# Kernel optimization log

Measured on AMD Instinct MI355X. Metric: run time of the kernel, lower is better.

Reference implementation:

```python
import jax, jax.numpy as jnp
import numpy as np

N_HEAD = 16
MA_K = 0.02          # sigmoid temperature in ma_k_activation
LEAKY_SLOPE = 0.02   # negative_slope in ma_q_activation
NEG_INF = -1e9


def setup_inputs() -> dict:
    key = jax.random.key(0)
    k1, k2, k3, k4 = jax.random.split(key, 4)
    B, T, C = 2, 2048, 1024
    x = jax.random.normal(k1, (B, T, C), dtype=jnp.float32)
    s = 1.0 / np.sqrt(C)
    W_attn = jax.random.normal(k2, (C, 2 * C), dtype=jnp.float32) * s
    W_k2 = jax.random.normal(k3, (C, C), dtype=jnp.float32) * s
    W_proj = jax.random.normal(k4, (C, C), dtype=jnp.float32) * s
    return {"x": x, "W_attn": W_attn, "W_k2": W_k2, "W_proj": W_proj}


def _heads(t, H):
    # [B,T,C] -> [B,H,T,d]
    B, T, C = t.shape
    return t.reshape(B, T, H, C // H).transpose(0, 2, 1, 3)


def reference(x, W_attn, W_k2, W_proj):
    B, T, C = x.shape
    H = N_HEAD
    d = C // H
    scale = 1.0 / jnp.sqrt(jnp.asarray(d, x.dtype))

    qk = x @ W_attn                      # [B,T,2C]
    q, k = jnp.split(qk, 2, axis=-1)
    q = _heads(q, H)                     # [B,H,T,d]
    k = _heads(k, H)
    v = _heads(x, H)                     # v = x

    # --- AR branch: causal softmax attention ---
    scores = jnp.einsum('bhtd,bhsd->bhts', q, k) * scale
    causal = jnp.tril(jnp.ones((T, T), dtype=bool))
    scores = jnp.where(causal, scores, NEG_INF)
    attn = jax.nn.softmax(scores, axis=-1)
    y = jnp.einsum('bhts,bhsd->bhtd', attn, v)   # [B,H,T,d]

    # --- MA branch: causal, softmax-free linear attention on residual ---
    e = v[:, :, 1:, :] - y[:, :, :-1, :]          # [B,H,T-1,d]
    k2 = _heads(x[:, :-1, :] @ W_k2, H)           # [B,H,T-1,d]
    q2 = q[:, :, 1:, :]                           # [B,H,T-1,d]

    qa = -jax.nn.leaky_relu(-q2 * scale, negative_slope=LEAKY_SLOPE)
    ka = jax.nn.sigmoid(MA_K * (k2 * scale))

    w = jnp.einsum('bhtd,bhsd->bhts', qa, ka)     # [B,H,T-1,T-1]
    w = jnp.tril(w)
    y2 = jnp.einsum('bhts,bhsd->bhtd', w, e)      # [B,H,T-1,d]
    y2 = jnp.concatenate([jnp.zeros_like(y2[:, :, :1, :]), y2], axis=2)  # pad front

    def merge(t):  # [B,H,T,d] -> [B,T,C]
        return t.transpose(0, 2, 1, 3).reshape(B, T, C)

    return merge(y) @ W_proj + merge(y2) @ W_proj
```

## Files before the change

### kernel.cpp

```cpp
#include <hip/hip_runtime.h>

typedef unsigned short u16;
typedef u16   u16x4  __attribute__((ext_vector_type(4)));
typedef u16   u16x8  __attribute__((ext_vector_type(8)));
typedef __bf16 bf16x8 __attribute__((ext_vector_type(8)));
typedef float  f32x4  __attribute__((ext_vector_type(4)));

__device__ __forceinline__ float bf2f(u16 v) {
    unsigned u = ((unsigned)v) << 16;
    return __builtin_bit_cast(float, u);
}
__device__ __forceinline__ u16 f2bf(float f) {
    unsigned u = __builtin_bit_cast(unsigned, f);
    u += 0x7fffu + ((u >> 16) & 1u);
    return (u16)(u >> 16);
}

__device__ __forceinline__ void async16(const u16* g, u16* l) {
    __builtin_amdgcn_global_load_lds(
        (const __attribute__((address_space(1))) unsigned int*)g,
        (__attribute__((address_space(3))) unsigned int*)l,
        16, 0, 0);
}

__device__ __forceinline__ size_t kimg_idx(int bh, int s, int d) {
    return ((size_t)(bh * 32 + (s >> 6)) * 4096) + (size_t)(((d >> 3) * 64 + (s & 63)) * 8) + (d & 7);
}
__device__ __forceinline__ size_t vimg_idx(int bh, int s, int d) {
    return ((size_t)(bh * 32 + (s >> 6)) * 4096) + (size_t)((((s & 63) >> 3) * 64 + d) * 8) + (s & 7);
}

__global__ __launch_bounds__(256)
void convert_pack(const float* __restrict__ in, u16* __restrict__ xb,
                  u16* __restrict__ xpack) {
    int i = blockIdx.x * 256 + threadIdx.x;
    int c4 = i & 255, row = i >> 8;
    int s = row & 2047, b = row >> 11;
    float4 v = ((const float4*)in)[i];
    u16x4 o;
    o.x = f2bf(v.x); o.y = f2bf(v.y); o.z = f2bf(v.z); o.w = f2bf(v.w);
    ((u16x4*)xb)[i] = o;
    int h = c4 >> 4, d0 = (c4 & 15) * 4;
    size_t base = vimg_idx(b * 16 + h, s, d0);
    xpack[base]      = o.x;
    xpack[base + 8]  = o.y;
    xpack[base + 16] = o.z;
    xpack[base + 24] = o.w;
}

__global__ __launch_bounds__(256)
void prep_weights(const float* __restrict__ Wa, const float* __restrict__ Wk,
                  const float* __restrict__ Wp, u16* __restrict__ Wta,
                  u16* __restrict__ Wtk, u16* __restrict__ Wtp) {
    __shared__ u16 tile[64][65];
    const int bx = blockIdx.x;
    const float* in; u16* out; int Cd, cx;
    if (bx < 32)      { in = Wa; out = Wta; Cd = 2048; cx = bx; }
    else if (bx < 48) { in = Wk; out = Wtk; Cd = 1024; cx = bx - 32; }
    else              { in = Wp; out = Wtp; Cd = 1024; cx = bx - 48; }
    const int c0 = cx * 64, r0 = blockIdx.y * 64;
    const int tid = threadIdx.x;
#pragma unroll
    for (int i = 0; i < 16; ++i) {
        int idx = tid + i * 256;
        int r = idx >> 6, c = idx & 63;
        tile[r][c] = f2bf(in[(size_t)(r0 + r) * Cd + c0 + c]);
    }
    __syncthreads();
#pragma unroll
    for (int i = 0; i < 16; ++i) {
        int idx = tid + i * 256;
        int r = idx >> 6, c = idx & 63;
        out[(size_t)(c0 + r) * 1024 + r0 + c] = tile[c][r];
    }
}

__global__ __launch_bounds__(256, 3)
void gemm_fused(const u16* __restrict__ A, const u16* __restrict__ Bt,
                u16* __restrict__ qs, u16* __restrict__ kpack,
                u16* __restrict__ kapack) {
    const int K = 1024;
    __shared__ __align__(16) u16 As[4][128][8];
    __shared__ __align__(16) u16 Bs[4][128][8];
    const int tid = threadIdx.x;
    const int wave = tid >> 6, lane = tid & 63;
    const int m0 = blockIdx.y * 128, n0 = blockIdx.x * 128;
    const int wm = (wave >> 1) * 64, wn = (wave & 1) * 64;
    const int q = lane >> 4, mr = lane & 15;

    const int s0 = tid, s1 = 256 + tid;
    const u16* gA0 = A  + (size_t)(m0 + (s0 & 127)) * K + (s0 >> 7) * 8;
    const u16* gA1 = A  + (size_t)(m0 + (s1 & 127)) * K + (s1 >> 7) * 8;
    const u16* gB0 = Bt + (size_t)(n0 + (s0 & 127)) * K + (s0 >> 7) * 8;
    const u16* gB1 = Bt + (size_t)(n0 + (s1 & 127)) * K + (s1 >> 7) * 8;
    u16* lA0 = &As[0][0][0] + (size_t)s0 * 8;
    u16* lA1 = &As[0][0][0] + (size_t)s1 * 8;
    u16* lB0 = &Bs[0][0][0] + (size_t)s0 * 8;
    u16* lB1 = &Bs[0][0][0] + (size_t)s1 * 8;

    f32x4 acc[4][4];
#pragma unroll
    for (int i = 0; i < 4; ++i)
#pragma unroll
        for (int j = 0; j < 4; ++j) acc[i][j] = f32x4{0.f, 0.f, 0.f, 0.f};

    for (int k0 = 0; k0 < K; k0 += 32) {
        __syncthreads();
        async16(gA0 + k0, lA0);
        async16(gA1 + k0, lA1);
        async16(gB0 + k0, lB0);
        async16(gB1 + k0, lB1);
        asm volatile("s_waitcnt vmcnt(0)" ::: "memory");
        __syncthreads();
        bf16x8 af[4], bfr[4];
#pragma unroll
        for (int i = 0; i < 4; ++i) af[i]  = *(const bf16x8*)&As[q][wm + i * 16 + mr][0];
#pragma unroll
        for (int j = 0; j < 4; ++j) bfr[j] = *(const bf16x8*)&Bs[q][wn + j * 16 + mr][0];
#pragma unroll
        for (int i = 0; i < 4; ++i)
#pragma unroll
            for (int j = 0; j < 4; ++j)
                acc[i][j] = __builtin_amdgcn_mfma_f32_16x16x32_bf16(af[i], bfr[j], acc[i][j], 0, 0, 0);
    }
#pragma unroll
    for (int i = 0; i < 4; ++i)
#pragma unroll
        for (int j = 0; j < 4; ++j)
#pragma unroll
            for (int r = 0; r < 4; ++r) {
                int m = m0 + wm + i * 16 + q * 4 + r;
                int n = n0 + wn + j * 16 + mr;
                float v = acc[i][j][r];
                int b = m >> 11, s = m & 2047;
                if (n < 1024) {
                    qs[(size_t)m * 1024 + n] = f2bf(v * 0.125f);
                } else if (n < 2048) {
                    int nn = n - 1024;
                    kpack[kimg_idx(b * 16 + (nn >> 6), s, nn & 63)] = f2bf(v);
                } else {
                    int nn = n - 2048;
                    kapack[kimg_idx(b * 16 + (nn >> 6), s, nn & 63)] =
                        f2bf(1.f / (1.f + __expf(-0.0025f * v)));
                }
            }
}

__global__ __launch_bounds__(256, 2)
void gemm64(const u16* __restrict__ A, const u16* __restrict__ Bt,
            float* __restrict__ Cv, int N, int K) {
    __shared__ __align__(16) u16 As[4][64][8];
    __shared__ __align__(16) u16 Bs[4][128][8];
    const int tid = threadIdx.x;
    const int wave = tid >> 6, lane = tid & 63;
    const int m0 = blockIdx.y * 64, n0 = blockIdx.x * 128;
    const int wn0 = wave * 32;
    const int q = lane >> 4, mr = lane & 15;

    const u16* gA = A + (size_t)(m0 + (tid & 63)) * K + (tid >> 6) * 8;
    u16* lA = &As[0][0][0] + (size_t)tid * 8;
    const int s1 = 256 + tid;
    const u16* gB0 = Bt + (size_t)(n0 + (tid & 127)) * K + (tid >> 7) * 8;
    const u16* gB1 = Bt + (size_t)(n0 + (s1 & 127)) * K + (s1 >> 7) * 8;
    u16* lB0 = &Bs[0][0][0] + (size_t)tid * 8;
    u16* lB1 = &Bs[0][0][0] + (size_t)s1 * 8;

    f32x4 acc[4][2];
#pragma unroll
    for (int i = 0; i < 4; ++i)
#pragma unroll
        for (int j = 0; j < 2; ++j) acc[i][j] = f32x4{0.f, 0.f, 0.f, 0.f};

    for (int k0 = 0; k0 < K; k0 += 32) {
        __syncthreads();
        async16(gA + k0, lA);
        async16(gB0 + k0, lB0);
        async16(gB1 + k0, lB1);
        asm volatile("s_waitcnt vmcnt(0)" ::: "memory");
        __syncthreads();
        bf16x8 af[4], bfr[2];
#pragma unroll
        for (int i = 0; i < 4; ++i) af[i]  = *(const bf16x8*)&As[q][i * 16 + mr][0];
#pragma unroll
        for (int j = 0; j < 2; ++j) bfr[j] = *(const bf16x8*)&Bs[q][wn0 + j * 16 + mr][0];
#pragma unroll
        for (int i = 0; i < 4; ++i)
#pragma unroll
            for (int j = 0; j < 2; ++j)
                acc[i][j] = __builtin_amdgcn_mfma_f32_16x16x32_bf16(af[i], bfr[j], acc[i][j], 0, 0, 0);
    }
#pragma unroll
    for (int i = 0; i < 4; ++i)
#pragma unroll
        for (int j = 0; j < 2; ++j)
#pragma unroll
            for (int r = 0; r < 4; ++r) {
                int m = m0 + i * 16 + q * 4 + r;
                int n = n0 + wn0 + j * 16 + mr;
                Cv[(size_t)m * N + n] = acc[i][j][r];
            }
}

__global__ __launch_bounds__(256, 2)
void flash_mfma(const u16* __restrict__ qs, const u16* __restrict__ kpack,
                const u16* __restrict__ xpack, u16* __restrict__ Opart,
                float* __restrict__ lpart) {
    __shared__ __align__(16) u16 Ks[8][64][8];
    __shared__ __align__(16) u16 Vs[8][64][8];
    __shared__ __align__(16) u16 Ps[4][16][72];
    const int bh = blockIdx.y, b = bh >> 4, hc = (bh & 15) * 64;
    const int z = blockIdx.z;
    const int tid = threadIdx.x, w = tid >> 6, lane = tid & 63;
    const int n16 = lane & 15, quad = lane >> 4;
    const u16* kbase = kpack + (size_t)bh * 32 * 4096;
    const u16* vbase = xpack + (size_t)bh * 32 * 4096;
    u16* Ob = Opart + (size_t)z * 4096 * 1024;
    float* lb = lpart + z * 65536;

    for (int rep = 0; rep < 2; ++rep) {
        const int T = rep ? 15 - (int)blockIdx.x : (int)blockIdx.x;
        const int t0 = T * 128;
        const int nchunk = 2 * T + 2;

        bf16x8 qf[2][2];
#pragma unroll
        for (int mt = 0; mt < 2; ++mt) {
            const int trow = t0 + (w + mt * 4) * 16 + n16;
            const u16* qp = &qs[(size_t)(b * 2048 + trow) * 1024 + hc + quad * 8];
            qf[mt][0] = *(const bf16x8*)qp;
            qf[mt][1] = *(const bf16x8*)(qp + 32);
        }

        f32x4 O[2][4];
        float lsum[2][4];
#pragma unroll
        for (int mt = 0; mt < 2; ++mt)
#pragma unroll
            for (int jt = 0; jt < 4; ++jt) { O[mt][jt] = f32x4{0.f, 0.f, 0.f, 0.f}; }
#pragma unroll
        for (int mt = 0; mt < 2; ++mt)
#pragma unroll
            for (int r = 0; r < 4; ++r) lsum[mt][r] = 0.f;

        u16x8 kr0, kr1, vr0, vr1;
        auto pref = [&](int c) {
            const u16* kc = kbase + (size_t)c * 4096;
            const u16* vc = vbase + (size_t)c * 4096;
            kr0 = *(const u16x8*)(kc + tid * 8);
            kr1 = *(const u16x8*)(kc + (256 + tid) * 8);
            vr0 = *(const u16x8*)(vc + tid * 8);
            vr1 = *(const u16x8*)(vc + (256 + tid) * 8);
        };
        if (z < nchunk) pref(z);

        for (int c = z; c < nchunk; c += 2) {
            __syncthreads();
            *(u16x8*)((u16*)Ks + tid * 8)         = kr0;
            *(u16x8*)((u16*)Ks + (256 + tid) * 8) = kr1;
            *(u16x8*)((u16*)Vs + tid * 8)         = vr0;
            *(u16x8*)((u16*)Vs + (256 + tid) * 8) = vr1;
            __syncthreads();
            if (c + 2 < nchunk) pref(c + 2);

            f32x4 S[2][4];
#pragma unroll
            for (int mt = 0; mt < 2; ++mt)
#pragma unroll
                for (int jt = 0; jt < 4; ++jt) S[mt][jt] = f32x4{0.f, 0.f, 0.f, 0.f};
#pragma unroll
            for (int ks = 0; ks < 2; ++ks)
#pragma unroll
                for (int jt = 0; jt < 4; ++jt) {
                    bf16x8 kf = *(const bf16x8*)&Ks[ks * 4 + quad][jt * 16 + n16][0];
                    S[0][jt] = __builtin_amdgcn_mfma_f32_16x16x32_bf16(qf[0][ks], kf, S[0][jt], 0, 0, 0);
                    S[1][jt] = __builtin_amdgcn_mfma_f32_16x16x32_bf16(qf[1][ks], kf, S[1][jt], 0, 0, 0);
                }
            bf16x8 vf[2][4];
#pragma unroll
            for (int ks = 0; ks < 2; ++ks)
#pragma unroll
                for (int jt = 0; jt < 4; ++jt)
                    vf[ks][jt] = *(const bf16x8*)&Vs[ks * 4 + quad][jt * 16 + n16][0];

#pragma unroll
            for (int mt = 0; mt < 2; ++mt) {
                if (mt == 0 && c == 2 * T + 1) continue;
                float p[4][4];
#pragma unroll
                for (int reg = 0; reg < 4; ++reg)
#pragma unroll
                    for (int jt = 0; jt < 4; ++jt)
                        p[reg][jt] = __expf(S[mt][jt][reg]);
                if (c == 2 * T + mt) {
#pragma unroll
                    for (int reg = 0; reg < 4; ++reg) {
                        const int tr = t0 + (w + mt * 4) * 16 + quad * 4 + reg;
#pragma unroll
                        for (int jt = 0; jt < 4; ++jt)
                            if (c * 64 + jt * 16 + n16 > tr) p[reg][jt] = 0.f;
                    }
                }
#pragma unroll
                for (int reg = 0; reg < 4; ++reg) {
                    lsum[mt][reg] += (p[reg][0] + p[reg][1]) + (p[reg][2] + p[reg][3]);
#pragma unroll
                    for (int jt = 0; jt < 4; ++jt)
                        Ps[w][quad * 4 + reg][jt * 16 + n16] = f2bf(p[reg][jt]);
                }
                bf16x8 pf[2];
#pragma unroll
                for (int ks = 0; ks < 2; ++ks)
                    pf[ks] = *(const bf16x8*)&Ps[w][n16][ks * 32 + quad * 8];
#pragma unroll
                for (int ks = 0; ks < 2; ++ks)
#pragma unroll
                    for (int jt = 0; jt < 4; ++jt)
                        O[mt][jt] = __builtin_amdgcn_mfma_f32_16x16x32_bf16(pf[ks], vf[ks][jt], O[mt][jt], 0, 0, 0);
            }
        }

#pragma unroll
        for (int mt = 0; mt < 2; ++mt)
#pragma unroll
            for (int reg = 0; reg < 4; ++reg) {
                float l = lsum[mt][reg];
#pragma unroll
                for (int off = 1; off < 16; off <<= 1) l += __shfl_xor(l, off, 64);
                const int tr = t0 + (w + mt * 4) * 16 + quad * 4 + reg;
                if (n16 == 0) lb[bh * 2048 + tr] = l;
                const size_t row = (size_t)(b * 2048 + tr) * 1024 + hc;
#pragma unroll
                for (int jt = 0; jt < 4; ++jt)
                    Ob[row + jt * 16 + n16] = f2bf(O[mt][jt][reg]);
            }
    }
}

__global__ __launch_bounds__(256)
void combine_flash(const u16* __restrict__ Opart, const float* __restrict__ lpart,
                   const u16* __restrict__ xb, u16* __restrict__ y,
                   u16* __restrict__ epack) {
    int i = blockIdx.x * 256 + threadIdx.x;
    int c4 = i & 255, row = i >> 8, t = row & 2047, b = row >> 11;
    int h = c4 >> 4, d0 = (c4 & 15) * 4;
    size_t off = (size_t)row * 1024 + c4 * 4;
    u16x4 o0 = *(const u16x4*)&Opart[off];
    u16x4 o1 = *(const u16x4*)&Opart[(size_t)4096 * 1024 + off];
    int lrow = (b * 16 + h) * 2048 + t;
    float inv = 1.f / (lpart[lrow] + lpart[65536 + lrow]);
    float y0 = (bf2f(o0.x) + bf2f(o1.x)) * inv;
    float y1 = (bf2f(o0.y) + bf2f(o1.y)) * inv;
    float y2 = (bf2f(o0.z) + bf2f(o1.z)) * inv;
    float y3 = (bf2f(o0.w) + bf2f(o1.w)) * inv;
    u16x4 yo;
    yo.x = f2bf(y0); yo.y = f2bf(y1); yo.z = f2bf(y2); yo.w = f2bf(y3);
    *(u16x4*)&y[off] = yo;
    float e0 = 0.f, e1 = 0.f, e2 = 0.f, e3 = 0.f;
    if (t < 2047) {
        u16x4 xv = *(const u16x4*)&xb[off + 1024];
        e0 = bf2f(xv.x) - y0; e1 = bf2f(xv.y) - y1;
        e2 = bf2f(xv.z) - y2; e3 = bf2f(xv.w) - y3;
    }
    size_t base = vimg_idx(b * 16 + h, t, d0);
    epack[base]      = f2bf(e0);
    epack[base + 8]  = f2bf(e1);
    epack[base + 16] = f2bf(e2);
    epack[base + 24] = f2bf(e3);
}

__global__ __launch_bounds__(256, 2)
void arma_mfma(const u16* __restrict__ qs, const u16* __restrict__ kapack,
               const u16* __restrict__ epack, u16* __restrict__ Opart) {
    __shared__ __align__(16) u16 Ks[8][64][8];
    __shared__ __align__(16) u16 Es[8][64][8];
    __shared__ __align__(16) u16 Ps[4][16][72];
    const int bh = blockIdx.y, b = bh >> 4, hc = (bh & 15) * 64;
    const int z = blockIdx.z;
    const int tid = threadIdx.x, w = tid >> 6, lane = tid & 63;
    const int n16 = lane & 15, quad = lane >> 4;
    const u16* kbase = kapack + (size_t)bh * 32 * 4096;
    const u16* vbase = epack + (size_t)bh * 32 * 4096;
    u16* Ob = Opart + (size_t)z * 4096 * 1024;

    for (int rep = 0; rep < 2; ++rep) {
        const int T = rep ? 15 - (int)blockIdx.x : (int)blockIdx.x;
        const int t0 = T * 128;
        const int nchunk = 2 * T + 2;

        bf16x8 qf[2][2];
#pragma unroll
        for (int mt = 0; mt < 2; ++mt) {
            const int trow = t0 + (w + mt * 4) * 16 + n16;
            const u16* qp = &qs[(size_t)(b * 2048 + trow) * 1024 + hc + quad * 8];
#pragma unroll
            for (int ks = 0; ks < 2; ++ks) {
                u16x8 qv = *(const u16x8*)(qp + ks * 32);
                u16x8 o;
#pragma unroll
                for (int j = 0; j < 8; ++j) {
                    float zv = bf2f(qv[j]);
                    o[j] = f2bf(zv < 0.f ? zv : 0.02f * zv);
                }
                qf[mt][ks] = __builtin_bit_cast(bf16x8, o);
            }
        }

        f32x4 O[2][4];
#pragma unroll
        for (int mt = 0; mt < 2; ++mt)
#pragma unroll
            for (int jt = 0; jt < 4; ++jt) O[mt][jt] = f32x4{0.f, 0.f, 0.f, 0.f};

        u16x8 kr0, kr1, vr0, vr1;
        auto pref = [&](int c) {
            const u16* kc = kbase + (size_t)c * 4096;
            const u16* vc = vbase + (size_t)c * 4096;
            kr0 = *(const u16x8*)(kc + tid * 8);
            kr1 = *(const u16x8*)(kc + (256 + tid) * 8);
            vr0 = *(const u16x8*)(vc + tid * 8);
            vr1 = *(const u16x8*)(vc + (256 + tid) * 8);
        };
        if (z < nchunk) pref(z);

        for (int c = z; c < nchunk; c += 2) {
            __syncthreads();
            *(u16x8*)((u16*)Ks + tid * 8)         = kr0;
            *(u16x8*)((u16*)Ks + (256 + tid) * 8) = kr1;
            *(u16x8*)((u16*)Es + tid * 8)         = vr0;
            *(u16x8*)((u16*)Es + (256 + tid) * 8) = vr1;
            __syncthreads();
            if (c + 2 < nchunk) pref(c + 2);

            f32x4 S[2][4];
#pragma unroll
            for (int mt = 0; mt < 2; ++mt)
#pragma unroll
                for (int jt = 0; jt < 4; ++jt) S[mt][jt] = f32x4{0.f, 0.f, 0.f, 0.f};
#pragma unroll
            for (int ks = 0; ks < 2; ++ks)
#pragma unroll
                for (int jt = 0; jt < 4; ++jt) {
                    bf16x8 kf = *(const bf16x8*)&Ks[ks * 4 + quad][jt * 16 + n16][0];
                    S[0][jt] = __builtin_amdgcn_mfma_f32_16x16x32_bf16(qf[0][ks], kf, S[0][jt], 0, 0, 0);
                    S[1][jt] = __builtin_amdgcn_mfma_f32_16x16x32_bf16(qf[1][ks], kf, S[1][jt], 0, 0, 0);
                }
            bf16x8 vf[2][4];
#pragma unroll
            for (int ks = 0; ks < 2; ++ks)
#pragma unroll
                for (int jt = 0; jt < 4; ++jt)
                    vf[ks][jt] = *(const bf16x8*)&Es[ks * 4 + quad][jt * 16 + n16][0];

#pragma unroll
            for (int mt = 0; mt < 2; ++mt) {
                if (mt == 0 && c == 2 * T + 1) continue;
                if (c == 2 * T + mt) {
#pragma unroll
                    for (int reg = 0; reg < 4; ++reg) {
                        const int tr = t0 + (w + mt * 4) * 16 + quad * 4 + reg;
#pragma unroll
                        for (int jt = 0; jt < 4; ++jt)
                            if (c * 64 + jt * 16 + n16 >= tr) S[mt][jt][reg] = 0.f;
                    }
                }
#pragma unroll
                for (int reg = 0; reg < 4; ++reg)
#pragma unroll
                    for (int jt = 0; jt < 4; ++jt)
                        Ps[w][quad * 4 + reg][jt * 16 + n16] = f2bf(S[mt][jt][reg]);
                bf16x8 pf[2];
#pragma unroll
                for (int ks = 0; ks < 2; ++ks)
                    pf[ks] = *(const bf16x8*)&Ps[w][n16][ks * 32 + quad * 8];
#pragma unroll
                for (int ks = 0; ks < 2; ++ks)
#pragma unroll
                    for (int jt = 0; jt < 4; ++jt)
                        O[mt][jt] = __builtin_amdgcn_mfma_f32_16x16x32_bf16(pf[ks], vf[ks][jt], O[mt][jt], 0, 0, 0);
            }
        }

#pragma unroll
        for (int mt = 0; mt < 2; ++mt)
#pragma unroll
            for (int reg = 0; reg < 4; ++reg) {
                const int tr = t0 + (w + mt * 4) * 16 + quad * 4 + reg;
                const size_t row = (size_t)(b * 2048 + tr) * 1024 + hc;
#pragma unroll
                for (int jt = 0; jt < 4; ++jt)
                    Ob[row + jt * 16 + n16] = f2bf(O[mt][jt][reg]);
            }
    }
}

__global__ __launch_bounds__(256)
void combine_arma(const u16* __restrict__ Opart, const u16* __restrict__ y,
                  u16* __restrict__ ys) {
    int i = blockIdx.x * 256 + threadIdx.x;
    size_t off = (size_t)i * 4;
    u16x4 o0 = *(const u16x4*)&Opart[off];
    u16x4 o1 = *(const u16x4*)&Opart[(size_t)4096 * 1024 + off];
    u16x4 yv = *(const u16x4*)&y[off];
    u16x4 r;
    r.x = f2bf(bf2f(yv.x) + bf2f(o0.x) + bf2f(o1.x));
    r.y = f2bf(bf2f(yv.y) + bf2f(o0.y) + bf2f(o1.y));
    r.z = f2bf(bf2f(yv.z) + bf2f(o0.z) + bf2f(o1.z));
    r.w = f2bf(bf2f(yv.w) + bf2f(o0.w) + bf2f(o1.w));
    *(u16x4*)&ys[off] = r;
}

extern "C" void kernel_launch(void* const* d_in, const int* in_sizes, int n_in,
                              void* d_out, int out_size, void* d_ws, size_t ws_size,
                              hipStream_t stream) {
    const float* x      = (const float*)d_in[0];
    const float* W_attn = (const float*)d_in[1];
    const float* W_k2   = (const float*)d_in[2];
    const float* W_proj = (const float*)d_in[3];
    float* out = (float*)d_out;

    char* w = (char*)d_ws;
    u16* xb      = (u16*)w; w += (size_t)4096 * 1024 * 2;
    u16* Wt_attn = (u16*)w; w += (size_t)2048 * 1024 * 2;
    u16* Wt_k2   = (u16*)w; w += (size_t)1024 * 1024 * 2;
    u16* Wt_proj = (u16*)w; w += (size_t)1024 * 1024 * 2;
    u16* qs      = (u16*)w; w += (size_t)4096 * 1024 * 2;
    u16* kpack   = (u16*)w; w += (size_t)4096 * 1024 * 2;
    u16* kapack  = (u16*)w; w += (size_t)4096 * 1024 * 2;
    u16* xpack   = (u16*)w; w += (size_t)4096 * 1024 * 2;
    u16* y       = (u16*)w; w += (size_t)4096 * 1024 * 2;
    u16* epack   = (u16*)w; w += (size_t)4096 * 1024 * 2;
    u16* Opart   = (u16*)w; w += (size_t)2 * 4096 * 1024 * 2;
    float* lpart = (float*)w; w += (size_t)2 * 65536 * 4;
    u16* ys = xb;

    convert_pack<<<dim3(4096), dim3(256), 0, stream>>>(x, xb, xpack);
    prep_weights<<<dim3(64, 16), dim3(256), 0, stream>>>(W_attn, W_k2, W_proj,
                                                         Wt_attn, Wt_k2, Wt_proj);
    gemm_fused<<<dim3(24, 32), dim3(256), 0, stream>>>(xb, Wt_attn, qs, kpack, kapack);
    flash_mfma<<<dim3(8, 32, 2), dim3(256), 0, stream>>>(qs, kpack, xpack, Opart, lpart);
    combine_flash<<<dim3(4096), dim3(256), 0, stream>>>(Opart, lpart, xb, y, epack);
    arma_mfma<<<dim3(8, 32, 2), dim3(256), 0, stream>>>(qs, kapack, epack, Opart);
    combine_arma<<<dim3(4096), dim3(256), 0, stream>>>(Opart, y, ys);
    gemm64<<<dim3(8, 64), dim3(256), 0, stream>>>(ys, Wt_proj, out, 1024, 1024);
}
```

Baseline: 296.6 us.

## Double-buffer LDS tiles in both GEMM kernels to overlap loads with MFMA

Both bf16 GEMM kernels now keep two shared-memory buffers for each K-step. The next tile's async global-to-LDS load is issued before the MFMA work on the current tile, which should hide global load latency behind compute and drop one barrier per iteration. In exchange LDS use per block doubles, which could lower occupancy, and the wait at the end of each step still serializes on the loads.

```diff
diff --git a/kernel.cpp b/kernel.cpp
--- a/kernel.cpp
+++ b/kernel.cpp
@@ -80,8 +80,8 @@
                 u16* __restrict__ qs, u16* __restrict__ kpack,
                 u16* __restrict__ kapack) {
     const int K = 1024;
-    __shared__ __align__(16) u16 As[4][128][8];
-    __shared__ __align__(16) u16 Bs[4][128][8];
+    __shared__ __align__(16) u16 As[2][4][128][8];
+    __shared__ __align__(16) u16 Bs[2][4][128][8];
     const int tid = threadIdx.x;
     const int wave = tid >> 6, lane = tid & 63;
     const int m0 = blockIdx.y * 128, n0 = blockIdx.x * 128;
@@ -93,10 +93,9 @@
     const u16* gA1 = A  + (size_t)(m0 + (s1 & 127)) * K + (s1 >> 7) * 8;
     const u16* gB0 = Bt + (size_t)(n0 + (s0 & 127)) * K + (s0 >> 7) * 8;
     const u16* gB1 = Bt + (size_t)(n0 + (s1 & 127)) * K + (s1 >> 7) * 8;
-    u16* lA0 = &As[0][0][0] + (size_t)s0 * 8;
-    u16* lA1 = &As[0][0][0] + (size_t)s1 * 8;
-    u16* lB0 = &Bs[0][0][0] + (size_t)s0 * 8;
-    u16* lB1 = &Bs[0][0][0] + (size_t)s1 * 8;
+    u16* const lA = &As[0][0][0][0];
+    u16* const lB = &Bs[0][0][0][0];
+    const int dA0 = s0 * 8, dA1 = s1 * 8;
 
     f32x4 acc[4][4];
 #pragma unroll
@@ -104,24 +103,36 @@
 #pragma unroll
         for (int j = 0; j < 4; ++j) acc[i][j] = f32x4{0.f, 0.f, 0.f, 0.f};
 
+    async16(gA0, lA + dA0);
+    async16(gA1, lA + dA1);
+    async16(gB0, lB + dA0);
+    async16(gB1, lB + dA1);
+    asm volatile("s_waitcnt vmcnt(0)" ::: "memory");
+    __syncthreads();
+
+    int cur = 0;
     for (int k0 = 0; k0 < K; k0 += 32) {
-        __syncthreads();
-        async16(gA0 + k0, lA0);
-        async16(gA1 + k0, lA1);
-        async16(gB0 + k0, lB0);
-        async16(gB1 + k0, lB1);
+        const int nxt = cur ^ 1;
+        if (k0 + 32 < K) {
+            const int kn = k0 + 32;
+            async16(gA0 + kn, lA + nxt * 4096 + dA0);
+            async16(gA1 + kn, lA + nxt * 4096 + dA1);
+            async16(gB0 + kn, lB + nxt * 4096 + dA0);
+            async16(gB1 + kn, lB + nxt * 4096 + dA1);
+        }
+        bf16x8 af[4], bfr[4];
+#pragma unroll
+        for (int i = 0; i < 4; ++i) af[i]  = *(const bf16x8*)&As[cur][q][wm + i * 16 + mr][0];
+#pragma unroll
+        for (int j = 0; j < 4; ++j) bfr[j] = *(const bf16x8*)&Bs[cur][q][wn + j * 16 + mr][0];
+#pragma unroll
+        for (int i = 0; i < 4; ++i)
+#pragma unroll
+            for (int j = 0; j < 4; ++j)
+                acc[i][j] = __builtin_amdgcn_mfma_f32_16x16x32_bf16(af[i], bfr[j], acc[i][j], 0, 0, 0);
         asm volatile("s_waitcnt vmcnt(0)" ::: "memory");
         __syncthreads();
-        bf16x8 af[4], bfr[4];
-#pragma unroll
-        for (int i = 0; i < 4; ++i) af[i]  = *(const bf16x8*)&As[q][wm + i * 16 + mr][0];
-#pragma unroll
-        for (int j = 0; j < 4; ++j) bfr[j] = *(const bf16x8*)&Bs[q][wn + j * 16 + mr][0];
-#pragma unroll
-        for (int i = 0; i < 4; ++i)
-#pragma unroll
-            for (int j = 0; j < 4; ++j)
-                acc[i][j] = __builtin_amdgcn_mfma_f32_16x16x32_bf16(af[i], bfr[j], acc[i][j], 0, 0, 0);
+        cur = nxt;
     }
 #pragma unroll
     for (int i = 0; i < 4; ++i)
@@ -149,8 +160,8 @@
 __global__ __launch_bounds__(256, 2)
 void gemm64(const u16* __restrict__ A, const u16* __restrict__ Bt,
             float* __restrict__ Cv, int N, int K) {
-    __shared__ __align__(16) u16 As[4][64][8];
-    __shared__ __align__(16) u16 Bs[4][128][8];
+    __shared__ __align__(16) u16 As[2][4][64][8];
+    __shared__ __align__(16) u16 Bs[2][4][128][8];
     const int tid = threadIdx.x;
     const int wave = tid >> 6, lane = tid & 63;
     const int m0 = blockIdx.y * 64, n0 = blockIdx.x * 128;
@@ -158,12 +169,12 @@
     const int q = lane >> 4, mr = lane & 15;
 
     const u16* gA = A + (size_t)(m0 + (tid & 63)) * K + (tid >> 6) * 8;
-    u16* lA = &As[0][0][0] + (size_t)tid * 8;
     const int s1 = 256 + tid;
     const u16* gB0 = Bt + (size_t)(n0 + (tid & 127)) * K + (tid >> 7) * 8;
     const u16* gB1 = Bt + (size_t)(n0 + (s1 & 127)) * K + (s1 >> 7) * 8;
-    u16* lB0 = &Bs[0][0][0] + (size_t)tid * 8;
-    u16* lB1 = &Bs[0][0][0] + (size_t)s1 * 8;
+    u16* const lA = &As[0][0][0][0];
+    u16* const lB = &Bs[0][0][0][0];
+    const int dA = tid * 8, dB0 = tid * 8, dB1 = s1 * 8;
 
     f32x4 acc[4][2];
 #pragma unroll
@@ -171,23 +182,34 @@
 #pragma unroll
         for (int j = 0; j < 2; ++j) acc[i][j] = f32x4{0.f, 0.f, 0.f, 0.f};
 
+    async16(gA, lA + dA);
+    async16(gB0, lB + dB0);
+    async16(gB1, lB + dB1);
+    asm volatile("s_waitcnt vmcnt(0)" ::: "memory");
+    __syncthreads();
+
+    int cur = 0;
     for (int k0 = 0; k0 < K; k0 += 32) {
-        __syncthreads();
-        async16(gA + k0, lA);
-        async16(gB0 + k0, lB0);
-        async16(gB1 + k0, lB1);
+        const int nxt = cur ^ 1;
+        if (k0 + 32 < K) {
+            const int kn = k0 + 32;
+            async16(gA + kn, lA + nxt * 2048 + dA);
+            async16(gB0 + kn, lB + nxt * 4096 + dB0);
+            async16(gB1 + kn, lB + nxt * 4096 + dB1);
+        }
+        bf16x8 af[4], bfr[2];
+#pragma unroll
+        for (int i = 0; i < 4; ++i) af[i]  = *(const bf16x8*)&As[cur][q][i * 16 + mr][0];
+#pragma unroll
+        for (int j = 0; j < 2; ++j) bfr[j] = *(const bf16x8*)&Bs[cur][q][wn0 + j * 16 + mr][0];
+#pragma unroll
+        for (int i = 0; i < 4; ++i)
+#pragma unroll
+            for (int j = 0; j < 2; ++j)
+                acc[i][j] = __builtin_amdgcn_mfma_f32_16x16x32_bf16(af[i], bfr[j], acc[i][j], 0, 0, 0);
         asm volatile("s_waitcnt vmcnt(0)" ::: "memory");
         __syncthreads();
-        bf16x8 af[4], bfr[2];
-#pragma unroll
-        for (int i = 0; i < 4; ++i) af[i]  = *(const bf16x8*)&As[q][i * 16 + mr][0];
-#pragma unroll
-        for (int j = 0; j < 2; ++j) bfr[j] = *(const bf16x8*)&Bs[q][wn0 + j * 16 + mr][0];
-#pragma unroll
-        for (int i = 0; i < 4; ++i)
-#pragma unroll
-            for (int j = 0; j < 2; ++j)
-                acc[i][j] = __builtin_amdgcn_mfma_f32_16x16x32_bf16(af[i], bfr[j], acc[i][j], 0, 0, 0);
+        cur = nxt;
     }
 #pragma unroll
     for (int i = 0; i < 4; ++i)
```

Result: no change. 291.6 us (-1.7%).

## Triple-buffer LDS tiles in projection GEMMs with two-stage async prefetch

Applied to the files above, without the earlier changes.

Both GEMM kernels (the fused QK/K2 projection and the output projection) now use three LDS buffers and issue async global-to-LDS loads two K-steps ahead. Each iteration waits only on the older batch with a partial vmcnt, and one barrier replaces the previous two. This aims to hide global load latency behind the MFMA work instead of stalling on every tile. LDS use per block triples, which may limit occupancy.

```diff
diff --git a/kernel.cpp b/kernel.cpp
--- a/kernel.cpp
+++ b/kernel.cpp
@@ -79,9 +79,9 @@
 void gemm_fused(const u16* __restrict__ A, const u16* __restrict__ Bt,
                 u16* __restrict__ qs, u16* __restrict__ kpack,
                 u16* __restrict__ kapack) {
-    const int K = 1024;
-    __shared__ __align__(16) u16 As[4][128][8];
-    __shared__ __align__(16) u16 Bs[4][128][8];
+    const int K = 1024, NT = K / 32;
+    __shared__ __align__(16) u16 As[3][4][128][8];
+    __shared__ __align__(16) u16 Bs[3][4][128][8];
     const int tid = threadIdx.x;
     const int wave = tid >> 6, lane = tid & 63;
     const int m0 = blockIdx.y * 128, n0 = blockIdx.x * 128;
@@ -93,10 +93,9 @@
     const u16* gA1 = A  + (size_t)(m0 + (s1 & 127)) * K + (s1 >> 7) * 8;
     const u16* gB0 = Bt + (size_t)(n0 + (s0 & 127)) * K + (s0 >> 7) * 8;
     const u16* gB1 = Bt + (size_t)(n0 + (s1 & 127)) * K + (s1 >> 7) * 8;
-    u16* lA0 = &As[0][0][0] + (size_t)s0 * 8;
-    u16* lA1 = &As[0][0][0] + (size_t)s1 * 8;
-    u16* lB0 = &Bs[0][0][0] + (size_t)s0 * 8;
-    u16* lB1 = &Bs[0][0][0] + (size_t)s1 * 8;
+    u16* const lA = &As[0][0][0][0];
+    u16* const lB = &Bs[0][0][0][0];
+    const int dA0 = s0 * 8, dA1 = s1 * 8;
 
     f32x4 acc[4][4];
 #pragma unroll
@@ -104,24 +103,42 @@
 #pragma unroll
         for (int j = 0; j < 4; ++j) acc[i][j] = f32x4{0.f, 0.f, 0.f, 0.f};
 
-    for (int k0 = 0; k0 < K; k0 += 32) {
+    async16(gA0,      lA + dA0);
+    async16(gA1,      lA + dA1);
+    async16(gB0,      lB + dA0);
+    async16(gB1,      lB + dA1);
+    async16(gA0 + 32, lA + 4096 + dA0);
+    async16(gA1 + 32, lA + 4096 + dA1);
+    async16(gB0 + 32, lB + 4096 + dA0);
+    async16(gB1 + 32, lB + 4096 + dA1);
+
+    int co = 0;
+    int io = 2 * 4096;
+    for (int t = 0; t < NT; ++t) {
+        if (t < NT - 1) asm volatile("s_waitcnt vmcnt(4)" ::: "memory");
+        else            asm volatile("s_waitcnt vmcnt(0)" ::: "memory");
         __syncthreads();
-        async16(gA0 + k0, lA0);
-        async16(gA1 + k0, lA1);
-        async16(gB0 + k0, lB0);
-        async16(gB1 + k0, lB1);
-        asm volatile("s_waitcnt vmcnt(0)" ::: "memory");
-        __syncthreads();
+        if (t + 2 < NT) {
+            const int kn = (t + 2) * 32;
+            async16(gA0 + kn, lA + io + dA0);
+            async16(gA1 + kn, lA + io + dA1);
+            async16(gB0 + kn, lB + io + dA0);
+            async16(gB1 + kn, lB + io + dA1);
+        }
         bf16x8 af[4], bfr[4];
 #pragma unroll
-        for (int i = 0; i < 4; ++i) af[i]  = *(const bf16x8*)&As[q][wm + i * 16 + mr][0];
-#pragma unroll
-        for (int j = 0; j < 4; ++j) bfr[j] = *(const bf16x8*)&Bs[q][wn + j * 16 + mr][0];
+        for (int i = 0; i < 4; ++i)
+            af[i]  = *(const bf16x8*)(lA + co + (size_t)(q * 128 + wm + i * 16 + mr) * 8);
+#pragma unroll
+        for (int j = 0; j < 4; ++j)
+            bfr[j] = *(const bf16x8*)(lB + co + (size_t)(q * 128 + wn + j * 16 + mr) * 8);
 #pragma unroll
         for (int i = 0; i < 4; ++i)
 #pragma unroll
             for (int j = 0; j < 4; ++j)
                 acc[i][j] = __builtin_amdgcn_mfma_f32_16x16x32_bf16(af[i], bfr[j], acc[i][j], 0, 0, 0);
+        co += 4096; if (co == 3 * 4096) co = 0;
+        io += 4096; if (io == 3 * 4096) io = 0;
     }
 #pragma unroll
     for (int i = 0; i < 4; ++i)
@@ -149,8 +166,9 @@
 __global__ __launch_bounds__(256, 2)
 void gemm64(const u16* __restrict__ A, const u16* __restrict__ Bt,
             float* __restrict__ Cv, int N, int K) {
-    __shared__ __align__(16) u16 As[4][64][8];
-    __shared__ __align__(16) u16 Bs[4][128][8];
+    const int NT = K / 32;
+    __shared__ __align__(16) u16 As[3][4][64][8];
+    __shared__ __align__(16) u16 Bs[3][4][128][8];
     const int tid = threadIdx.x;
     const int wave = tid >> 6, lane = tid & 63;
     const int m0 = blockIdx.y * 64, n0 = blockIdx.x * 128;
@@ -158,12 +176,12 @@
     const int q = lane >> 4, mr = lane & 15;
 
     const u16* gA = A + (size_t)(m0 + (tid & 63)) * K + (tid >> 6) * 8;
-    u16* lA = &As[0][0][0] + (size_t)tid * 8;
     const int s1 = 256 + tid;
     const u16* gB0 = Bt + (size_t)(n0 + (tid & 127)) * K + (tid >> 7) * 8;
     const u16* gB1 = Bt + (size_t)(n0 + (s1 & 127)) * K + (s1 >> 7) * 8;
-    u16* lB0 = &Bs[0][0][0] + (size_t)tid * 8;
-    u16* lB1 = &Bs[0][0][0] + (size_t)s1 * 8;
+    u16* const lA = &As[0][0][0][0];
+    u16* const lB = &Bs[0][0][0][0];
+    const int dA = tid * 8, dB0 = tid * 8, dB1 = s1 * 8;
 
     f32x4 acc[4][2];
 #pragma unroll
@@ -171,23 +189,40 @@
 #pragma unroll
         for (int j = 0; j < 2; ++j) acc[i][j] = f32x4{0.f, 0.f, 0.f, 0.f};
 
-    for (int k0 = 0; k0 < K; k0 += 32) {
+    async16(gA,       lA + dA);
+    async16(gB0,      lB + dB0);
+    async16(gB1,      lB + dB1);
+    async16(gA + 32,  lA + 2048 + dA);
+    async16(gB0 + 32, lB + 4096 + dB0);
+    async16(gB1 + 32, lB + 4096 + dB1);
+
+    int coA = 0, coB = 0, ioA = 2 * 2048, ioB = 2 * 4096;
+    for (int t = 0; t < NT; ++t) {
+        if (t < NT - 1) asm volatile("s_waitcnt vmcnt(3)" ::: "memory");
+        else            asm volatile("s_waitcnt vmcnt(0)" ::: "memory");
         __syncthreads();
-        async16(gA + k0, lA);
-        async16(gB0 + k0, lB0);
-        async16(gB1 + k0, lB1);
-        asm volatile("s_waitcnt vmcnt(0)" ::: "memory");
-        __syncthreads();
+        if (t + 2 < NT) {
+            const int kn = (t + 2) * 32;
+            async16(gA + kn,  lA + ioA + dA);
+            async16(gB0 + kn, lB + ioB + dB0);
+            async16(gB1 + kn, lB + ioB + dB1);
+        }
         bf16x8 af[4], bfr[2];
 #pragma unroll
-        for (int i = 0; i < 4; ++i) af[i]  = *(const bf16x8*)&As[q][i * 16 + mr][0];
-#pragma unroll
-        for (int j = 0; j < 2; ++j) bfr[j] = *(const bf16x8*)&Bs[q][wn0 + j * 16 + mr][0];
+        for (int i = 0; i < 4; ++i)
+            af[i]  = *(const bf16x8*)(lA + coA + (size_t)(q * 64 + i * 16 + mr) * 8);
+#pragma unroll
+        for (int j = 0; j < 2; ++j)
+            bfr[j] = *(const bf16x8*)(lB + coB + (size_t)(q * 128 + wn0 + j * 16 + mr) * 8);
 #pragma unroll
         for (int i = 0; i < 4; ++i)
 #pragma unroll
             for (int j = 0; j < 2; ++j)
                 acc[i][j] = __builtin_amdgcn_mfma_f32_16x16x32_bf16(af[i], bfr[j], acc[i][j], 0, 0, 0);
+        coA += 2048; if (coA == 3 * 2048) coA = 0;
+        coB += 4096; if (coB == 3 * 4096) coB = 0;
+        ioA += 2048; if (ioA == 3 * 2048) ioA = 0;
+        ioB += 4096; if (ioB == 3 * 4096) ioB = 0;
     }
 #pragma unroll
     for (int i = 0; i < 4; ++i)
```

Measured after the change: 294.9 us. Within noise of the previous version (-0.6%).
